# Kernel optimization log

Measured on AMD Instinct MI355X. Metric: run time of the kernel, lower is better.

The kernel has to match this reference:

```python
import jax, jax.numpy as jnp
import numpy as np
import math

N_OBS, DIM_IN, DIM_HIDDEN = 2048, 64, 1024
LENGTHSCALE = 1.0


def setup_inputs() -> dict:
    key = jax.random.key(0)
    kx, kw, kb = jax.random.split(key, 3)
    x = jax.random.normal(kx, (N_OBS, DIM_IN), dtype=jnp.float32)
    # buffer w ~ Normal(0, 1/lengthscale), b ~ Uniform(0, 2*pi)
    w = jax.random.normal(kw, (DIM_HIDDEN, DIM_IN), dtype=jnp.float32) / LENGTHSCALE
    b = jax.random.uniform(kb, (DIM_HIDDEN,), dtype=jnp.float32, minval=0.0, maxval=2.0 * math.pi)
    return {"x": x, "w": w, "b": b}


def reference(x, w, b):
    """compute_Ax: analytic jacobian of hidden_features + per-dim Gram matrices.

    hidden h = sqrt(2/K) * cos(x @ w.T + b)
    jacobian J[n,k,d] = -sqrt(2/K) * sin(z[n,k]) * w[k,d]
    A_d[k,l] = (1/n) * sum_n J[n,k,d] * J[n,l,d]
             = (1/n) * (S^T S)[k,l] * w[k,d] * w[l,d],  S = -sqrt(2/K) sin(z)
    Returns A stacked: (dim_in, K, K).
    """
    n = x.shape[0]
    K = w.shape[0]
    scale = math.sqrt(2.0 / K)
    z = x @ w.T + b  # (n, K)
    s = (-scale) * jnp.sin(z)  # (n, K)
    M = (s.T @ s) / n  # (K, K) shared Gram of sin-activations
    # A[d,k,l] = M[k,l] * w[k,d] * w[l,d]
    A = jnp.einsum('kl,kd,ld->dkl', M, w, w)
    return A
```

## Files before the change

### kernel.cpp

```cpp
#include <hip/hip_runtime.h>
#include <math.h>

#define N_OBS   2048
#define DIM_IN  64
#define K_HID   1024
#define NSPLIT  2
#define NT_CHUNK ((N_OBS / NSPLIT) / 64)

typedef unsigned short ushort_t;
typedef __attribute__((ext_vector_type(8))) short bf16x8;
typedef __attribute__((ext_vector_type(4))) float f32x4;

__device__ __forceinline__ ushort_t f2bf(float f) {
    unsigned int u = __float_as_uint(f);
    u += 0x7FFF + ((u >> 16) & 1);
    return (ushort_t)(u >> 16);
}

#define GLD_LDS16(g, l)                                                   \
    __builtin_amdgcn_global_load_lds(                                     \
        (const __attribute__((address_space(1))) void*)(g),               \
        (__attribute__((address_space(3))) void*)(l), 16, 0, 0)

__global__ __launch_bounds__(256) void rff_compute_s(
    const float* __restrict__ x, const float* __restrict__ w,
    const float* __restrict__ b, ushort_t* __restrict__ sT,
    float* __restrict__ wt) {
    __shared__ float xs[16][64];
    __shared__ float wT[64][65];

    const int t  = threadIdx.x;
    const int k0 = blockIdx.x * 64;
    const int n0 = blockIdx.y * 16;

    {
        int r = t >> 4, c = (t & 15) * 4;
        *(float4*)&xs[r][c] = *(const float4*)(x + (n0 + r) * DIM_IN + c);
    }
#pragma unroll
    for (int i = 0; i < 4; ++i) {
        int r = (t >> 4) + 16 * i, c = (t & 15) * 4;
        float4 v = *(const float4*)(w + (k0 + r) * DIM_IN + c);
        wT[c + 0][r] = v.x; wT[c + 1][r] = v.y;
        wT[c + 2][r] = v.z; wT[c + 3][r] = v.w;
    }
    __syncthreads();

    const int k  = t & 63;
    const int nb = t >> 6;

    if (blockIdx.y == 0) {
#pragma unroll
        for (int dd = 0; dd < 16; ++dd) {
            const int d = nb + dd * 4;
            wt[d * K_HID + k0 + k] = wT[d][k];
        }
    }

    const float bk = b[k0 + k];
    float z[4];
#pragma unroll
    for (int i = 0; i < 4; ++i) z[i] = bk;

    for (int d4 = 0; d4 < 64; d4 += 4) {
        float xv[4][4];
#pragma unroll
        for (int i = 0; i < 4; ++i)
            *(float4*)xv[i] = *(const float4*)&xs[nb * 4 + i][d4];
#pragma unroll
        for (int j = 0; j < 4; ++j) {
            const float wv = wT[d4 + j][k];
#pragma unroll
            for (int i = 0; i < 4; ++i) z[i] += xv[i][j] * wv;
        }
    }

    const float scale = 0.04419417382415922f;
    ushort4 ov;
    ov.x = f2bf(-scale * __sinf(z[0]));
    ov.y = f2bf(-scale * __sinf(z[1]));
    ov.z = f2bf(-scale * __sinf(z[2]));
    ov.w = f2bf(-scale * __sinf(z[3]));
    *(ushort4*)(sT + (size_t)(k0 + k) * N_OBS + n0 + nb * 4) = ov;
}

__device__ __forceinline__ void stage_tiles(
    const ushort_t* __restrict__ sT, ushort_t* lA, ushort_t* lB,
    int k0, int l0, int ncol0, int wv, int srow, int sslot) {
#pragma unroll
    for (int j = 0; j < 2; ++j) {
        const int c = wv * 2 + j;
        const ushort_t* gA = sT + (size_t)(k0 + c * 8 + srow) * N_OBS + ncol0 + sslot * 8;
        const ushort_t* gB = sT + (size_t)(l0 + c * 8 + srow) * N_OBS + ncol0 + sslot * 8;
        GLD_LDS16(gA, lA + c * 512);
        GLD_LDS16(gB, lB + c * 512);
    }
}

__global__ __launch_bounds__(256) void rff_gram_mfma(
    const ushort_t* __restrict__ sT, float* __restrict__ Mp) {
    __shared__ ushort_t ldsA[2][64 * 64];
    __shared__ ushort_t ldsB[2][64 * 64];

    const int t    = threadIdx.x;
    const int lane = t & 63;
    const int wv   = t >> 6;
    const int wr   = wv >> 1, wc = wv & 1;
    const int k0   = blockIdx.y * 64, l0 = blockIdx.x * 64;
    const int nbase = blockIdx.z * (N_OBS / NSPLIT);

    const int srow  = lane >> 3;
    const int sslot = (lane & 7) ^ srow;

    f32x4 acc[2][2];
#pragma unroll
    for (int a = 0; a < 2; ++a)
#pragma unroll
        for (int bb = 0; bb < 2; ++bb)
            acc[a][bb] = (f32x4){0.f, 0.f, 0.f, 0.f};

    const int rlo = lane & 15;
    const int hi  = lane >> 4;
    const int rx  = rlo & 7;

    stage_tiles(sT, &ldsA[0][0], &ldsB[0][0], k0, l0, nbase, wv, srow, sslot);
    __syncthreads();

    int cur = 0;
    for (int it = 0; it < NT_CHUNK; ++it) {
        if (it + 1 < NT_CHUNK)
            stage_tiles(sT, &ldsA[cur ^ 1][0], &ldsB[cur ^ 1][0],
                        k0, l0, nbase + (it + 1) * 64, wv, srow, sslot);
#pragma unroll
        for (int ks = 0; ks < 2; ++ks) {
            const int slot = (ks * 4 + hi) ^ rx;
            bf16x8 af[2], bfr[2];
#pragma unroll
            for (int a = 0; a < 2; ++a) {
                af[a]  = *(const bf16x8*)(&ldsA[cur][(wr * 32 + a * 16 + rlo) * 64 + slot * 8]);
                bfr[a] = *(const bf16x8*)(&ldsB[cur][(wc * 32 + a * 16 + rlo) * 64 + slot * 8]);
            }
#pragma unroll
            for (int a = 0; a < 2; ++a)
#pragma unroll
                for (int bb = 0; bb < 2; ++bb)
                    acc[a][bb] = __builtin_amdgcn_mfma_f32_16x16x32_bf16(
                        af[a], bfr[bb], acc[a][bb], 0, 0, 0);
        }
        __syncthreads();
        cur ^= 1;
    }

    float* Mz = Mp + (size_t)blockIdx.z * K_HID * K_HID;
    const int col = lane & 15;
    const int rq  = (lane >> 4) * 4;
#pragma unroll
    for (int a = 0; a < 2; ++a)
#pragma unroll
        for (int bb = 0; bb < 2; ++bb)
#pragma unroll
            for (int r = 0; r < 4; ++r) {
                const int row = k0 + wr * 32 + a * 16 + rq + r;
                const int cl  = l0 + wc * 32 + bb * 16 + col;
                Mz[(size_t)row * K_HID + cl] = acc[a][bb][r];
            }
}

__global__ __launch_bounds__(256) void rff_reduce_M(
    const float* __restrict__ Mp, float* __restrict__ M) {
    const int i = (blockIdx.x * 256 + threadIdx.x) * 4;
    const f32x4 a = *(const f32x4*)(Mp + i);
    const f32x4 c = *(const f32x4*)(Mp + (size_t)K_HID * K_HID + i);
    const float inv_n = 1.0f / (float)N_OBS;
    f32x4 o;
#pragma unroll
    for (int j = 0; j < 4; ++j) o[j] = (a[j] + c[j]) * inv_n;
    *(f32x4*)(M + i) = o;
}

__global__ __launch_bounds__(256) void rff_expand_A(
    const float* __restrict__ M, const float* __restrict__ wt,
    float* __restrict__ out) {
    const int kg = blockIdx.x;
    const int d  = blockIdx.y;
    const int t  = threadIdx.x;

    const f32x4 wl = *(const f32x4*)(wt + d * K_HID + t * 4);
    const int k0 = kg * 16;
#pragma unroll
    for (int i = 0; i < 16; ++i) {
        const int k = k0 + i;
        const float wk = wt[d * K_HID + k];
        const f32x4 mv = *(const f32x4*)(M + (size_t)k * K_HID + t * 4);
        f32x4 o;
#pragma unroll
        for (int j = 0; j < 4; ++j) o[j] = mv[j] * wk * wl[j];
        __builtin_nontemporal_store(
            o, (f32x4*)(out + ((size_t)(d * K_HID + k)) * K_HID + t * 4));
    }
}

extern "C" void kernel_launch(void* const* d_in, const int* in_sizes, int n_in,
                              void* d_out, int out_size, void* d_ws, size_t ws_size,
                              hipStream_t stream) {
    const float* x = (const float*)d_in[0];
    const float* w = (const float*)d_in[1];
    const float* b = (const float*)d_in[2];
    float* out = (float*)d_out;

    char* ws = (char*)d_ws;
    ushort_t* sT_buf = (ushort_t*)ws;
    float*    Mp_buf = (float*)(ws + (size_t)4  * 1024 * 1024);
    float*    M_buf  = (float*)(ws + (size_t)12 * 1024 * 1024);
    float*    wt_buf = (float*)(ws + (size_t)16 * 1024 * 1024);

    rff_compute_s<<<dim3(K_HID / 64, N_OBS / 16), 256, 0, stream>>>(x, w, b, sT_buf, wt_buf);
    rff_gram_mfma<<<dim3(K_HID / 64, K_HID / 64, NSPLIT), 256, 0, stream>>>(sT_buf, Mp_buf);
    rff_reduce_M<<<dim3(K_HID * K_HID / 1024), 256, 0, stream>>>(Mp_buf, M_buf);
    rff_expand_A<<<dim3(K_HID / 16, DIM_IN), 256, 0, stream>>>(M_buf, wt_buf, out);
}
```

Baseline: 301.8 us.

## Fuse Gram computation with A expansion and drop split-N reduction

Merges the Gram MFMA kernel, the partial-sum reduce kernel and the expansion kernel into one kernel. Each 64x64 tile of M is kept in LDS, scaled by 1/n, and expanded straight into all 64 output slices using w rows staged in LDS. This removes the M partial buffers, the reduce pass, the wt buffer and two launches. The cost is halved grid parallelism for the Gram step (256 blocks with a full-length N loop) and larger LDS use per block. The output write, which dominates traffic, is now issued from only 256 blocks.

```diff
diff --git a/kernel.cpp b/kernel.cpp
--- a/kernel.cpp
+++ b/kernel.cpp
@@ -4,8 +4,7 @@
 #define N_OBS   2048
 #define DIM_IN  64
 #define K_HID   1024
-#define NSPLIT  2
-#define NT_CHUNK ((N_OBS / NSPLIT) / 64)
+#define NCHUNK  (N_OBS / 64)
 
 typedef unsigned short ushort_t;
 typedef __attribute__((ext_vector_type(8))) short bf16x8;
@@ -24,8 +23,7 @@
 
 __global__ __launch_bounds__(256) void rff_compute_s(
     const float* __restrict__ x, const float* __restrict__ w,
-    const float* __restrict__ b, ushort_t* __restrict__ sT,
-    float* __restrict__ wt) {
+    const float* __restrict__ b, ushort_t* __restrict__ sT) {
     __shared__ float xs[16][64];
     __shared__ float wT[64][65];
 
@@ -48,15 +46,6 @@
 
     const int k  = t & 63;
     const int nb = t >> 6;
-
-    if (blockIdx.y == 0) {
-#pragma unroll
-        for (int dd = 0; dd < 16; ++dd) {
-            const int d = nb + dd * 4;
-            wt[d * K_HID + k0 + k] = wT[d][k];
-        }
-    }
-
     const float bk = b[k0 + k];
     float z[4];
 #pragma unroll
@@ -97,17 +86,21 @@
     }
 }
 
-__global__ __launch_bounds__(256) void rff_gram_mfma(
-    const ushort_t* __restrict__ sT, float* __restrict__ Mp) {
-    __shared__ ushort_t ldsA[2][64 * 64];
-    __shared__ ushort_t ldsB[2][64 * 64];
+__global__ __launch_bounds__(256) void rff_gram_expand(
+    const ushort_t* __restrict__ sT, const float* __restrict__ w,
+    float* __restrict__ out) {
+    __shared__ __align__(16) char smem[52224];
+    ushort_t* ldsA  = (ushort_t*)smem;
+    ushort_t* ldsB  = (ushort_t*)(smem + 16384);
+    float*    M_lds = (float*)smem;
+    float*    wkT   = (float*)(smem + 17408);
+    float*    wlT   = (float*)(smem + 34816);
 
     const int t    = threadIdx.x;
     const int lane = t & 63;
     const int wv   = t >> 6;
     const int wr   = wv >> 1, wc = wv & 1;
     const int k0   = blockIdx.y * 64, l0 = blockIdx.x * 64;
-    const int nbase = blockIdx.z * (N_OBS / NSPLIT);
 
     const int srow  = lane >> 3;
     const int sslot = (lane & 7) ^ srow;
@@ -123,22 +116,24 @@
     const int hi  = lane >> 4;
     const int rx  = rlo & 7;
 
-    stage_tiles(sT, &ldsA[0][0], &ldsB[0][0], k0, l0, nbase, wv, srow, sslot);
+    stage_tiles(sT, ldsA, ldsB, k0, l0, 0, wv, srow, sslot);
     __syncthreads();
 
     int cur = 0;
-    for (int it = 0; it < NT_CHUNK; ++it) {
-        if (it + 1 < NT_CHUNK)
-            stage_tiles(sT, &ldsA[cur ^ 1][0], &ldsB[cur ^ 1][0],
-                        k0, l0, nbase + (it + 1) * 64, wv, srow, sslot);
+    for (int it = 0; it < NCHUNK; ++it) {
+        if (it + 1 < NCHUNK)
+            stage_tiles(sT, ldsA + (cur ^ 1) * 4096, ldsB + (cur ^ 1) * 4096,
+                        k0, l0, (it + 1) * 64, wv, srow, sslot);
 #pragma unroll
         for (int ks = 0; ks < 2; ++ks) {
             const int slot = (ks * 4 + hi) ^ rx;
             bf16x8 af[2], bfr[2];
 #pragma unroll
             for (int a = 0; a < 2; ++a) {
-                af[a]  = *(const bf16x8*)(&ldsA[cur][(wr * 32 + a * 16 + rlo) * 64 + slot * 8]);
-                bfr[a] = *(const bf16x8*)(&ldsB[cur][(wc * 32 + a * 16 + rlo) * 64 + slot * 8]);
+                af[a]  = *(const bf16x8*)(ldsA + cur * 4096
+                          + (wr * 32 + a * 16 + rlo) * 64 + slot * 8);
+                bfr[a] = *(const bf16x8*)(ldsB + cur * 4096
+                          + (wc * 32 + a * 16 + rlo) * 64 + slot * 8);
             }
 #pragma unroll
             for (int a = 0; a < 2; ++a)
@@ -151,7 +146,7 @@
         cur ^= 1;
     }
 
-    float* Mz = Mp + (size_t)blockIdx.z * K_HID * K_HID;
+    const float inv_n = 1.0f / (float)N_OBS;
     const int col = lane & 15;
     const int rq  = (lane >> 4) * 4;
 #pragma unroll
@@ -160,43 +155,43 @@
         for (int bb = 0; bb < 2; ++bb)
 #pragma unroll
             for (int r = 0; r < 4; ++r) {
-                const int row = k0 + wr * 32 + a * 16 + rq + r;
-                const int cl  = l0 + wc * 32 + bb * 16 + col;
-                Mz[(size_t)row * K_HID + cl] = acc[a][bb][r];
+                const int row = wr * 32 + a * 16 + rq + r;
+                const int cl  = wc * 32 + bb * 16 + col;
+                M_lds[row * 68 + cl] = acc[a][bb][r] * inv_n;
             }
-}
-
-__global__ __launch_bounds__(256) void rff_reduce_M(
-    const float* __restrict__ Mp, float* __restrict__ M) {
-    const int i = (blockIdx.x * 256 + threadIdx.x) * 4;
-    const f32x4 a = *(const f32x4*)(Mp + i);
-    const f32x4 c = *(const f32x4*)(Mp + (size_t)K_HID * K_HID + i);
-    const float inv_n = 1.0f / (float)N_OBS;
-    f32x4 o;
-#pragma unroll
-    for (int j = 0; j < 4; ++j) o[j] = (a[j] + c[j]) * inv_n;
-    *(f32x4*)(M + i) = o;
-}
-
-__global__ __launch_bounds__(256) void rff_expand_A(
-    const float* __restrict__ M, const float* __restrict__ wt,
-    float* __restrict__ out) {
-    const int kg = blockIdx.x;
-    const int d  = blockIdx.y;
-    const int t  = threadIdx.x;
-
-    const f32x4 wl = *(const f32x4*)(wt + d * K_HID + t * 4);
-    const int k0 = kg * 16;
-#pragma unroll
-    for (int i = 0; i < 16; ++i) {
-        const int k = k0 + i;
-        const float wk = wt[d * K_HID + k];
-        const f32x4 mv = *(const f32x4*)(M + (size_t)k * K_HID + t * 4);
-        f32x4 o;
-#pragma unroll
-        for (int j = 0; j < 4; ++j) o[j] = mv[j] * wk * wl[j];
-        __builtin_nontemporal_store(
-            o, (f32x4*)(out + ((size_t)(d * K_HID + k)) * K_HID + t * 4));
+#pragma unroll
+    for (int i = 0; i < 4; ++i) {
+        const int r = (t >> 4) + 16 * i, c = (t & 15) * 4;
+        float4 vk = *(const float4*)(w + (k0 + r) * DIM_IN + c);
+        float4 vl = *(const float4*)(w + (l0 + r) * DIM_IN + c);
+        wkT[(c + 0) * 68 + r] = vk.x; wkT[(c + 1) * 68 + r] = vk.y;
+        wkT[(c + 2) * 68 + r] = vk.z; wkT[(c + 3) * 68 + r] = vk.w;
+        wlT[(c + 0) * 68 + r] = vl.x; wlT[(c + 1) * 68 + r] = vl.y;
+        wlT[(c + 2) * 68 + r] = vl.z; wlT[(c + 3) * 68 + r] = vl.w;
+    }
+    __syncthreads();
+
+    const int prow = t >> 4;
+    const int pcol = (t & 15) * 4;
+    f32x4 mv[4];
+#pragma unroll
+    for (int rr = 0; rr < 4; ++rr)
+        mv[rr] = *(const f32x4*)&M_lds[(rr * 16 + prow) * 68 + pcol];
+
+    float* outb = out + (size_t)k0 * K_HID + l0;
+    for (int d = 0; d < DIM_IN; ++d) {
+        const f32x4 wlv = *(const f32x4*)&wlT[d * 68 + pcol];
+        float* outd = outb + (size_t)d * K_HID * K_HID;
+#pragma unroll
+        for (int rr = 0; rr < 4; ++rr) {
+            const int row = rr * 16 + prow;
+            const float wk = wkT[d * 68 + row];
+            f32x4 o;
+#pragma unroll
+            for (int j = 0; j < 4; ++j) o[j] = mv[rr][j] * wk * wlv[j];
+            __builtin_nontemporal_store(
+                o, (f32x4*)(outd + (size_t)row * K_HID + pcol));
+        }
     }
 }
 
@@ -208,14 +203,8 @@
     const float* b = (const float*)d_in[2];
     float* out = (float*)d_out;
 
-    char* ws = (char*)d_ws;
-    ushort_t* sT_buf = (ushort_t*)ws;
-    float*    Mp_buf = (float*)(ws + (size_t)4  * 1024 * 1024);
-    float*    M_buf  = (float*)(ws + (size_t)12 * 1024 * 1024);
-    float*    wt_buf = (float*)(ws + (size_t)16 * 1024 * 1024);
-
-    rff_compute_s<<<dim3(K_HID / 64, N_OBS / 16), 256, 0, stream>>>(x, w, b, sT_buf, wt_buf);
-    rff_gram_mfma<<<dim3(K_HID / 64, K_HID / 64, NSPLIT), 256, 0, stream>>>(sT_buf, Mp_buf);
-    rff_reduce_M<<<dim3(K_HID * K_HID / 1024), 256, 0, stream>>>(Mp_buf, M_buf);
-    rff_expand_A<<<dim3(K_HID / 16, DIM_IN), 256, 0, stream>>>(M_buf, wt_buf, out);
-}
+    ushort_t* sT_buf = (ushort_t*)d_ws;
+
+    rff_compute_s<<<dim3(K_HID / 64, N_OBS / 16), 256, 0, stream>>>(x, w, b, sT_buf);
+    rff_gram_expand<<<dim3(K_HID / 64, K_HID / 64), 256, 0, stream>>>(sT_buf, w, out);
+}
```

Result: no change. 296.6 us (-1.8%).
